# Performance work log

Measured on AMD Instinct MI355X. Metric: run time of the kernel, lower is better.

Reference implementation:

```python
import jax, jax.numpy as jnp
import numpy as np

B, C, H, W = 2, 512, 64, 64
NUM_HEADS = 8
HEAD_DIM = C // NUM_HEADS


def setup_inputs() -> dict:
    key = jax.random.key(0)
    ks = jax.random.split(key, 6)
    s = 1.0 / np.sqrt(C)
    return {
        "x": jax.random.normal(ks[0], (B, C, H, W), dtype=jnp.float32),
        "w_qkv": jax.random.normal(ks[1], (3 * C, C), dtype=jnp.float32) * s,
        "b_qkv": jax.random.normal(ks[2], (3 * C,), dtype=jnp.float32) * 0.01,
        "w_out": jax.random.normal(ks[3], (C, C), dtype=jnp.float32) * s,
        "b_out": jax.random.normal(ks[4], (C,), dtype=jnp.float32) * 0.01,
        "gamma": jax.random.normal(ks[5], (1,), dtype=jnp.float32) * 0.1,
    }


def reference(x, w_qkv, b_qkv, w_out, b_out, gamma):
    b, c, h, w = x.shape
    n = h * w
    nh, hd = NUM_HEADS, HEAD_DIM
    # 1x1 conv QKV projection == per-pixel linear
    qkv = jnp.einsum('oc,bchw->bohw', w_qkv, x) + b_qkv[None, :, None, None]
    qkv = qkv.reshape(b, 3, nh, hd, n)  # [B,3,nh,hd,N]
    q = qkv[:, 0].transpose(0, 1, 3, 2)  # [B,nh,N,hd]
    k = qkv[:, 1]                        # [B,nh,hd,N]
    v = qkv[:, 2].transpose(0, 1, 3, 2)  # [B,nh,N,hd]
    scale = hd ** -0.5
    attn = jnp.einsum('bhnd,bhdm->bhnm', q, k) * scale  # [B,nh,N,N]
    attn = jax.nn.softmax(attn, axis=-1)
    out = jnp.einsum('bhnm,bhmd->bhnd', attn, v)  # [B,nh,N,hd]
    out = out.transpose(0, 1, 3, 2).reshape(b, c, h, w)  # [B,C,H,W]
    out = jnp.einsum('oc,bchw->bohw', w_out, out) + b_out[None, :, None, None]
    return gamma[0] * out + x
```

## Files before the change

kernel.cpp:

```cpp
#include <hip/hip_runtime.h>
#include <hip/hip_bf16.h>

typedef __bf16 bf16_t;
typedef __bf16 bf16x8 __attribute__((ext_vector_type(8)));
typedef __bf16 bf16x4 __attribute__((ext_vector_type(4)));
typedef float floatx4 __attribute__((ext_vector_type(4)));
typedef float f32x16 __attribute__((ext_vector_type(16)));

#define MFMA_BF16(a, b, c) __builtin_amdgcn_mfma_f32_16x16x32_bf16((a), (b), (c), 0, 0, 0)
#define MFMA32(a, b, c) __builtin_amdgcn_mfma_f32_32x32x16_bf16((a), (b), (c), 0, 0, 0)

static constexpr int CB = 512;
static constexpr int NB = 4096;

__device__ __forceinline__ unsigned cvtpk_bf16(float lo, float hi_) {
  unsigned r;
  asm("v_cvt_pk_bf16_f32 %0, %1, %2" : "=v"(r) : "v"(lo), "v"(hi_));
  return r;
}
__device__ __forceinline__ void plswap(unsigned& x, unsigned& y) {
  asm volatile("v_permlane32_swap_b32 %0, %1" : "+v"(x), "+v"(y));
}
__device__ __forceinline__ float exp2_fast(float x) {
  float r;
  asm("v_exp_f32 %0, %1" : "=v"(r) : "v"(x));
  return r;
}

#define GLOAD_LDS16(gsrc, ldst)                                              \
  __builtin_amdgcn_global_load_lds(                                          \
      (const __attribute__((address_space(1))) void*)(gsrc),                 \
      (__attribute__((address_space(3))) void*)(ldst), 16, 0, 0)

__global__ __launch_bounds__(256) void k_transpose(const float* __restrict__ x,
                                                   bf16_t* __restrict__ xT) {
  __shared__ __align__(16) bf16_t T[64 * 72];
  const int t = threadIdx.x;
  const int b = blockIdx.z, c0 = blockIdx.y * 64, n0 = blockIdx.x * 64;
  {
    const int cl = t >> 4, nl = (t & 15) * 4;
#pragma unroll
    for (int p = 0; p < 4; ++p) {
      const int c = cl + p * 16;
      const float4 v = *reinterpret_cast<const float4*>(
          x + ((size_t)(b * CB + c0 + c) * NB) + n0 + nl);
      T[(nl + 0) * 72 + c] = (bf16_t)v.x;
      T[(nl + 1) * 72 + c] = (bf16_t)v.y;
      T[(nl + 2) * 72 + c] = (bf16_t)v.z;
      T[(nl + 3) * 72 + c] = (bf16_t)v.w;
    }
  }
  __syncthreads();
  {
    const int nr = t >> 2, ch = t & 3;
    bf16_t* op = xT + ((size_t)(b * NB + n0 + nr) * CB) + c0;
#pragma unroll
    for (int p = 0; p < 2; ++p) {
      bf16x8 v = *reinterpret_cast<const bf16x8*>(&T[nr * 72 + ch * 8 + p * 32]);
      *reinterpret_cast<bf16x8*>(op + ch * 8 + p * 32) = v;
    }
  }
}

__global__ __launch_bounds__(256) void k_qkv(const float* __restrict__ W,
                                             const float* __restrict__ bias,
                                             const bf16_t* __restrict__ xT,
                                             bf16_t* __restrict__ Qb,
                                             bf16_t* __restrict__ Kb,
                                             bf16_t* __restrict__ Vb) {
  __shared__ __align__(16) bf16_t As[128 * 40];
  __shared__ __align__(16) bf16_t Bs[128 * 40];
  const int t = threadIdx.x;
  const int lane = t & 63, wv = t >> 6;
  const int g = lane >> 4, c = lane & 15;
  const int wm = wv >> 1, wn = wv & 1;
  const int o0 = blockIdx.x * 128, n0 = blockIdx.y * 128;
  const int b = blockIdx.z;

  floatx4 acc[4][4] = {};

  const float* Ap = W + (size_t)o0 * CB;
  const bf16_t* Bp = xT + ((size_t)b * NB + n0) * CB;

  for (int kt = 0; kt < CB; kt += 32) {
    {
      const int row = t >> 3, c4 = (t & 7) * 4;
#pragma unroll
      for (int p = 0; p < 4; ++p) {
        const int r = row + p * 32;
        const float4 v = *reinterpret_cast<const float4*>(Ap + (size_t)r * CB + kt + c4);
        bf16x4 w4;
        w4[0] = (bf16_t)v.x; w4[1] = (bf16_t)v.y; w4[2] = (bf16_t)v.z; w4[3] = (bf16_t)v.w;
        *reinterpret_cast<bf16x4*>(&As[r * 40 + c4]) = w4;
      }
    }
    {
      const int row = t >> 2, ch = t & 3;
#pragma unroll
      for (int p = 0; p < 2; ++p) {
        const int r = row + p * 64;
        bf16x8 v = *reinterpret_cast<const bf16x8*>(Bp + (size_t)r * CB + kt + ch * 8);
        *reinterpret_cast<bf16x8*>(&Bs[r * 40 + ch * 8]) = v;
      }
    }
    __syncthreads();
    bf16x8 af[4], bfr[4];
#pragma unroll
    for (int i = 0; i < 4; ++i)
      af[i] = *reinterpret_cast<const bf16x8*>(&As[(wm * 64 + i * 16 + c) * 40 + g * 8]);
#pragma unroll
    for (int j = 0; j < 4; ++j)
      bfr[j] = *reinterpret_cast<const bf16x8*>(&Bs[(wn * 64 + j * 16 + c) * 40 + g * 8]);
#pragma unroll
    for (int i = 0; i < 4; ++i)
#pragma unroll
      for (int j = 0; j < 4; ++j)
        acc[i][j] = MFMA_BF16(af[i], bfr[j], acc[i][j]);
    __syncthreads();
  }

  const int which = o0 >> 9;
#pragma unroll
  for (int i = 0; i < 4; ++i) {
    const int ob = o0 + wm * 64 + i * 16 + 4 * g;
    float bias4[4];
#pragma unroll
    for (int r = 0; r < 4; ++r) bias4[r] = bias[ob + r];
    const int h = (ob >> 6) & 7;
    const int d0 = ob & 63;
#pragma unroll
    for (int j = 0; j < 4; ++j) {
      const int n = n0 + wn * 64 + j * 16 + c;
      if (which == 2) {
        bf16_t* vp = Vb + (size_t)(b * 8 + h) * 64 * NB + n;
#pragma unroll
        for (int r = 0; r < 4; ++r)
          vp[(size_t)(d0 + r) * NB] = (bf16_t)(acc[i][j][r] + bias4[r]);
      } else {
        bf16_t* qp = (which == 0 ? Qb : Kb) + ((size_t)(b * 8 + h) * NB + n) * 64 + d0;
        bf16x4 pk;
#pragma unroll
        for (int r = 0; r < 4; ++r) pk[r] = (bf16_t)(acc[i][j][r] + bias4[r]);
        *reinterpret_cast<bf16x4*>(qp) = pk;
      }
    }
  }
}

__global__ __launch_bounds__(256, 3) void k_attn(const bf16_t* __restrict__ Qb,
                                                 const bf16_t* __restrict__ Kb,
                                                 const bf16_t* __restrict__ Vb,
                                                 bf16_t* __restrict__ P0,
                                                 bf16_t* __restrict__ P1,
                                                 float* __restrict__ lsum) {
  __shared__ __align__(16) bf16_t Kl[2][4096];
  __shared__ __align__(16) bf16_t Vl[2][4096];
  const int t = threadIdx.x, lane = t & 63, w = t >> 6;
  const int q31 = lane & 31, hi = lane >> 5;

  const int bid = blockIdx.x;
  const int xcd = bid & 7, j = bid >> 3;
  const int bh = xcd * 2 + (j >> 6);
  const int rest = j & 63;
  const int qt = rest >> 1, half = rest & 1;
  const int q0 = qt * 128 + w * 32;
  const int kvbase = half * 2048;

  const size_t base = (size_t)bh * NB * 64;
  const bf16_t* Qp = Qb + base;
  const bf16_t* Kp = Kb + base;
  const bf16_t* Vp = Vb + base;
  bf16_t* Op = (half ? P1 : P0) + base;

  const float SC = 0.125f * 1.44269504088896340736f;
  const float FM = 8.0f;

  bf16x8 qf[4];
#pragma unroll
  for (int ks = 0; ks < 4; ++ks) {
    bf16x8 q = *reinterpret_cast<const bf16x8*>(Qp + (size_t)(q0 + q31) * 64 + ks * 16 + hi * 8);
#pragma unroll
    for (int e = 0; e < 8; ++e) q[e] = (bf16_t)((float)q[e] * SC);
    qf[ks] = q;
  }

  bf16x8 ones;
#pragma unroll
  for (int e = 0; e < 8; ++e) ones[e] = (bf16_t)1.0f;

  const int srow0 = t >> 3, srow1 = srow0 + 32;
  const int sc0 = ((t & 7) ^ (srow0 & 7)) * 8;
  const int sc1 = ((t & 7) ^ (srow1 & 7)) * 8;
  const bf16_t* ksrc0 = Kp + (size_t)(kvbase + srow0) * 64 + sc0;
  const bf16_t* ksrc1 = Kp + (size_t)(kvbase + srow1) * 64 + sc1;
  const bf16_t* vsrc0 = Vp + (size_t)srow0 * NB + kvbase + sc0;
  const bf16_t* vsrc1 = Vp + (size_t)srow1 * NB + kvbase + sc1;

  int c16r[4];
#pragma unroll
  for (int ks = 0; ks < 4; ++ks) c16r[ks] = ((ks * 2 + hi) ^ (q31 & 7)) * 8;

  f32x16 O0 = {}, O1 = {}, lacc = {};
  f32x16 NEGM;
#pragma unroll
  for (int r = 0; r < 16; ++r) NEGM[r] = -FM;

  GLOAD_LDS16(ksrc0, &Kl[0][w * 512]);
  GLOAD_LDS16(ksrc1, &Kl[0][2048 + w * 512]);
  GLOAD_LDS16(vsrc0, &Vl[0][w * 512]);
  GLOAD_LDS16(vsrc1, &Vl[0][2048 + w * 512]);
  __syncthreads();

  for (int s = 0; s < 32; ++s) {
    const bf16_t* Kbuf = &Kl[s & 1][0];
    const bf16_t* Vbuf = &Vl[s & 1][0];
    if (s < 31) {
      const size_t ko = (size_t)(s + 1) * 64 * 64;
      const int vo = (s + 1) * 64;
      bf16_t* kd = &Kl[(s + 1) & 1][0];
      bf16_t* vd = &Vl[(s + 1) & 1][0];
      GLOAD_LDS16(ksrc0 + ko, kd + w * 512);
      GLOAD_LDS16(ksrc1 + ko, kd + 2048 + w * 512);
      GLOAD_LDS16(vsrc0 + vo, vd + w * 512);
      GLOAD_LDS16(vsrc1 + vo, vd + 2048 + w * 512);
    }
    f32x16 st0 = NEGM, st1 = NEGM;
    __builtin_amdgcn_s_setprio(1);
#pragma unroll
    for (int ks = 0; ks < 4; ++ks) {
      bf16x8 kf0 = *reinterpret_cast<const bf16x8*>(&Kbuf[q31 * 64 + c16r[ks]]);
      bf16x8 kf1 = *reinterpret_cast<const bf16x8*>(&Kbuf[(32 + q31) * 64 + c16r[ks]]);
      st0 = MFMA32(kf0, qf[ks], st0);
      st1 = MFMA32(kf1, qf[ks], st1);
    }
    __builtin_amdgcn_s_setprio(0);

#pragma unroll
    for (int r = 0; r < 16; ++r) st0[r] = exp2_fast(st0[r]);
#pragma unroll
    for (int r = 0; r < 16; ++r) st1[r] = exp2_fast(st1[r]);

    __builtin_amdgcn_s_setprio(1);
#pragma unroll
    for (int ks = 0; ks < 4; ++ks) {
      const f32x16& P = (ks < 2) ? st0 : st1;
      const int rb = (ks & 1) * 8;
      unsigned x0 = cvtpk_bf16(P[rb + 0], P[rb + 1]);
      unsigned y0 = cvtpk_bf16(P[rb + 4], P[rb + 5]);
      unsigned x1 = cvtpk_bf16(P[rb + 2], P[rb + 3]);
      unsigned y1 = cvtpk_bf16(P[rb + 6], P[rb + 7]);
      plswap(x0, y0);
      plswap(x1, y1);
      union { unsigned u[4]; bf16x8 v; } pa;
      pa.u[0] = x0; pa.u[1] = x1; pa.u[2] = y0; pa.u[3] = y1;
      bf16x8 vf0 = *reinterpret_cast<const bf16x8*>(&Vbuf[q31 * 64 + c16r[ks]]);
      bf16x8 vf1 = *reinterpret_cast<const bf16x8*>(&Vbuf[(32 + q31) * 64 + c16r[ks]]);
      O0 = MFMA32(pa.v, vf0, O0);
      O1 = MFMA32(pa.v, vf1, O1);
      lacc = MFMA32(pa.v, ones, lacc);
    }
    __builtin_amdgcn_s_setprio(0);
    __syncthreads();
  }

#pragma unroll
  for (int r = 0; r < 16; ++r) {
    const int n = q0 + (r & 3) + 8 * (r >> 2) + 4 * hi;
    bf16_t* op = Op + ((size_t)n) * 64 + q31;
    op[0]  = (bf16_t)O0[r];
    op[32] = (bf16_t)O1[r];
  }
  if (q31 == 0) {
    float* lp = lsum + (size_t)(half * 16 + bh) * NB;
#pragma unroll
    for (int r = 0; r < 16; ++r) {
      const int row = (r & 3) + 8 * (r >> 2) + 4 * hi;
      lp[q0 + row] = lacc[r];
    }
  }
}

__global__ __launch_bounds__(256) void k_rl(const float* __restrict__ lsum,
                                            float* __restrict__ rlb) {
  const int i = blockIdx.x * 256 + threadIdx.x;
  rlb[i] = 1.0f / (lsum[i] + lsum[i + 16 * NB]);
}

__global__ __launch_bounds__(256) void k_out(const float* __restrict__ W,
                                             const float* __restrict__ bias,
                                             const bf16_t* __restrict__ P0,
                                             const bf16_t* __restrict__ P1,
                                             const float* __restrict__ rlb,
                                             const float* __restrict__ x,
                                             const float* __restrict__ gamma,
                                             float* __restrict__ y) {
  __shared__ __align__(16) bf16_t As[128 * 40];
  __shared__ __align__(16) bf16_t Bs[128 * 40];
  const int t = threadIdx.x;
  const int lane = t & 63, wv = t >> 6;
  const int g = lane >> 4, c = lane & 15;
  const int wm = wv >> 1, wn = wv & 1;
  const int o0 = blockIdx.x * 128, n0 = blockIdx.y * 128;
  const int b = blockIdx.z;

  floatx4 acc[4][4] = {};

  const float* Ap = W + (size_t)o0 * CB;

  for (int kt = 0; kt < CB; kt += 32) {
    {
      const int row = t >> 3, c4 = (t & 7) * 4;
#pragma unroll
      for (int p = 0; p < 4; ++p) {
        const int r = row + p * 32;
        const float4 v = *reinterpret_cast<const float4*>(Ap + (size_t)r * CB + kt + c4);
        bf16x4 w4;
        w4[0] = (bf16_t)v.x; w4[1] = (bf16_t)v.y; w4[2] = (bf16_t)v.z; w4[3] = (bf16_t)v.w;
        *reinterpret_cast<bf16x4*>(&As[r * 40 + c4]) = w4;
      }
    }
    {
      const int row = t >> 2, ch = t & 3;
      const int cc = kt + ch * 8;
      const int h = cc >> 6, d = cc & 63;
#pragma unroll
      for (int p = 0; p < 2; ++p) {
        const int r = row + p * 64;
        const int n = n0 + r;
        const size_t idx = ((size_t)(b * 8 + h) * NB + n) * 64 + d;
        const bf16x8 oa = *reinterpret_cast<const bf16x8*>(P0 + idx);
        const bf16x8 ob = *reinterpret_cast<const bf16x8*>(P1 + idx);
        const float rl = rlb[(size_t)(b * 8 + h) * NB + n];
        bf16x8 o;
#pragma unroll
        for (int e = 0; e < 8; ++e)
          o[e] = (bf16_t)(((float)oa[e] + (float)ob[e]) * rl);
        *reinterpret_cast<bf16x8*>(&Bs[r * 40 + ch * 8]) = o;
      }
    }
    __syncthreads();
    bf16x8 af[4], bfr[4];
#pragma unroll
    for (int i = 0; i < 4; ++i)
      af[i] = *reinterpret_cast<const bf16x8*>(&As[(wm * 64 + i * 16 + c) * 40 + g * 8]);
#pragma unroll
    for (int j = 0; j < 4; ++j)
      bfr[j] = *reinterpret_cast<const bf16x8*>(&Bs[(wn * 64 + j * 16 + c) * 40 + g * 8]);
#pragma unroll
    for (int i = 0; i < 4; ++i)
#pragma unroll
      for (int j = 0; j < 4; ++j)
        acc[i][j] = MFMA_BF16(af[i], bfr[j], acc[i][j]);
    __syncthreads();
  }

  const float gm = gamma[0];
#pragma unroll
  for (int i = 0; i < 4; ++i) {
    const int ob = o0 + wm * 64 + i * 16 + 4 * g;
    float bias4[4];
#pragma unroll
    for (int r = 0; r < 4; ++r) bias4[r] = bias[ob + r];
#pragma unroll
    for (int j = 0; j < 4; ++j) {
      const int n = n0 + wn * 64 + j * 16 + c;
      const float* xp = x + ((size_t)(b * CB + ob) * NB) + n;
      float* yp = y + ((size_t)(b * CB + ob) * NB) + n;
#pragma unroll
      for (int r = 0; r < 4; ++r)
        yp[(size_t)r * NB] = gm * (acc[i][j][r] + bias4[r]) + xp[(size_t)r * NB];
    }
  }
}

extern "C" void kernel_launch(void* const* d_in, const int* in_sizes, int n_in,
                              void* d_out, int out_size, void* d_ws, size_t ws_size,
                              hipStream_t stream) {
  const float* x      = (const float*)d_in[0];
  const float* w_qkv  = (const float*)d_in[1];
  const float* b_qkv  = (const float*)d_in[2];
  const float* w_out  = (const float*)d_in[3];
  const float* b_out  = (const float*)d_in[4];
  const float* gamma  = (const float*)d_in[5];
  float* y = (float*)d_out;

  const size_t CH = 4194304;
  bf16_t* Wp = (bf16_t*)d_ws;
  bf16_t* Qb = Wp;
  bf16_t* Kb = Wp + CH;
  bf16_t* Vb = Wp + 2 * CH;
  bf16_t* P0 = Wp + 3 * CH;
  bf16_t* xT = Wp + 4 * CH;
  bf16_t* P1 = Wp + 4 * CH;
  float*  lsum = (float*)(Wp + 5 * CH);
  float*  rlb  = (float*)(Wp + 5 * CH + 262144 * 2);

  k_transpose<<<dim3(64, 8, 2), 256, 0, stream>>>(x, xT);
  k_qkv<<<dim3(12, 32, 2), 256, 0, stream>>>(w_qkv, b_qkv, xT, Qb, Kb, Vb);
  k_attn<<<dim3(1024), 256, 0, stream>>>(Qb, Kb, Vb, P0, P1, lsum);
  k_rl<<<dim3(256), 256, 0, stream>>>(lsum, rlb);
  k_out<<<dim3(4, 32, 2), 256, 0, stream>>>(w_out, b_out, P0, P1, rlb, x, gamma, y);
}
```

Baseline: 155.9 us.

## Triple-buffer K/V tiles in attention and fold reciprocal-sum kernel into output GEMM

The attention kernel moves from double- to triple-buffered K/V LDS tiles, prefetching two tiles ahead. It replaces __syncthreads with explicit vmcnt waits plus raw barriers, so one tile's loads can stay in flight across iterations. The separate k_rl launch is removed and k_out computes the reciprocal of the summed lsum partials inline. LDS per block rises from 32KB to 48KB, which may reduce occupancy at 3 blocks per CU, and the reciprocal is recomputed redundantly across output tiles.

After: 153.9 us. No clear change (-1.3%).

```diff
diff --git a/kernel.cpp b/kernel.cpp
--- a/kernel.cpp
+++ b/kernel.cpp
@@ -153,8 +153,8 @@
                                                  bf16_t* __restrict__ P0,
                                                  bf16_t* __restrict__ P1,
                                                  float* __restrict__ lsum) {
-  __shared__ __align__(16) bf16_t Kl[2][4096];
-  __shared__ __align__(16) bf16_t Vl[2][4096];
+  __shared__ __align__(16) bf16_t Kl[3][4096];
+  __shared__ __align__(16) bf16_t Vl[3][4096];
   const int t = threadIdx.x, lane = t & 63, w = t >> 6;
   const int q31 = lane & 31, hi = lane >> 5;
 
@@ -196,6 +196,18 @@
   const bf16_t* vsrc0 = Vp + (size_t)srow0 * NB + kvbase + sc0;
   const bf16_t* vsrc1 = Vp + (size_t)srow1 * NB + kvbase + sc1;
 
+#define STAGE_TILE(ss, slot)                                                  \
+  do {                                                                        \
+    const size_t ko_ = (size_t)(ss) * 64 * 64;                                \
+    const int vo_ = (ss) * 64;                                                \
+    bf16_t* kd_ = &Kl[(slot)][0];                                             \
+    bf16_t* vd_ = &Vl[(slot)][0];                                             \
+    GLOAD_LDS16(ksrc0 + ko_, kd_ + w * 512);                                  \
+    GLOAD_LDS16(ksrc1 + ko_, kd_ + 2048 + w * 512);                           \
+    GLOAD_LDS16(vsrc0 + vo_, vd_ + w * 512);                                  \
+    GLOAD_LDS16(vsrc1 + vo_, vd_ + 2048 + w * 512);                           \
+  } while (0)
+
   int c16r[4];
 #pragma unroll
   for (int ks = 0; ks < 4; ++ks) c16r[ks] = ((ks * 2 + hi) ^ (q31 & 7)) * 8;
@@ -205,24 +217,19 @@
 #pragma unroll
   for (int r = 0; r < 16; ++r) NEGM[r] = -FM;
 
-  GLOAD_LDS16(ksrc0, &Kl[0][w * 512]);
-  GLOAD_LDS16(ksrc1, &Kl[0][2048 + w * 512]);
-  GLOAD_LDS16(vsrc0, &Vl[0][w * 512]);
-  GLOAD_LDS16(vsrc1, &Vl[0][2048 + w * 512]);
-  __syncthreads();
-
+  STAGE_TILE(0, 0);
+  STAGE_TILE(1, 1);
+  asm volatile("s_waitcnt vmcnt(4)" ::: "memory");
+  __builtin_amdgcn_s_barrier();
+  __builtin_amdgcn_sched_barrier(0);
+
+  int cur = 0;
   for (int s = 0; s < 32; ++s) {
-    const bf16_t* Kbuf = &Kl[s & 1][0];
-    const bf16_t* Vbuf = &Vl[s & 1][0];
-    if (s < 31) {
-      const size_t ko = (size_t)(s + 1) * 64 * 64;
-      const int vo = (s + 1) * 64;
-      bf16_t* kd = &Kl[(s + 1) & 1][0];
-      bf16_t* vd = &Vl[(s + 1) & 1][0];
-      GLOAD_LDS16(ksrc0 + ko, kd + w * 512);
-      GLOAD_LDS16(ksrc1 + ko, kd + 2048 + w * 512);
-      GLOAD_LDS16(vsrc0 + vo, vd + w * 512);
-      GLOAD_LDS16(vsrc1 + vo, vd + 2048 + w * 512);
+    const bf16_t* Kbuf = &Kl[cur][0];
+    const bf16_t* Vbuf = &Vl[cur][0];
+    if (s < 30) {
+      int nx2 = cur + 2; if (nx2 >= 3) nx2 -= 3;
+      STAGE_TILE(s + 2, nx2);
     }
     f32x16 st0 = NEGM, st1 = NEGM;
     __builtin_amdgcn_s_setprio(1);
@@ -260,8 +267,18 @@
       lacc = MFMA32(pa.v, ones, lacc);
     }
     __builtin_amdgcn_s_setprio(0);
-    __syncthreads();
-  }
+
+    if (s < 31) {
+      if (s < 30)
+        asm volatile("s_waitcnt vmcnt(4) lgkmcnt(0)" ::: "memory");
+      else
+        asm volatile("s_waitcnt vmcnt(0) lgkmcnt(0)" ::: "memory");
+      __builtin_amdgcn_s_barrier();
+      __builtin_amdgcn_sched_barrier(0);
+    }
+    ++cur; if (cur >= 3) cur = 0;
+  }
+#undef STAGE_TILE
 
 #pragma unroll
   for (int r = 0; r < 16; ++r) {
@@ -280,17 +297,11 @@
   }
 }
 
-__global__ __launch_bounds__(256) void k_rl(const float* __restrict__ lsum,
-                                            float* __restrict__ rlb) {
-  const int i = blockIdx.x * 256 + threadIdx.x;
-  rlb[i] = 1.0f / (lsum[i] + lsum[i + 16 * NB]);
-}
-
 __global__ __launch_bounds__(256) void k_out(const float* __restrict__ W,
                                              const float* __restrict__ bias,
                                              const bf16_t* __restrict__ P0,
                                              const bf16_t* __restrict__ P1,
-                                             const float* __restrict__ rlb,
+                                             const float* __restrict__ lsum,
                                              const float* __restrict__ x,
                                              const float* __restrict__ gamma,
                                              float* __restrict__ y) {
@@ -327,10 +338,11 @@
       for (int p = 0; p < 2; ++p) {
         const int r = row + p * 64;
         const int n = n0 + r;
-        const size_t idx = ((size_t)(b * 8 + h) * NB + n) * 64 + d;
+        const size_t li = (size_t)(b * 8 + h) * NB + n;
+        const size_t idx = li * 64 + d;
         const bf16x8 oa = *reinterpret_cast<const bf16x8*>(P0 + idx);
         const bf16x8 ob = *reinterpret_cast<const bf16x8*>(P1 + idx);
-        const float rl = rlb[(size_t)(b * 8 + h) * NB + n];
+        const float rl = 1.0f / (lsum[li] + lsum[li + 16 * NB]);
         bf16x8 o;
 #pragma unroll
         for (int e = 0; e < 8; ++e)
@@ -393,11 +405,9 @@
   bf16_t* xT = Wp + 4 * CH;
   bf16_t* P1 = Wp + 4 * CH;
   float*  lsum = (float*)(Wp + 5 * CH);
-  float*  rlb  = (float*)(Wp + 5 * CH + 262144 * 2);
 
   k_transpose<<<dim3(64, 8, 2), 256, 0, stream>>>(x, xT);
   k_qkv<<<dim3(12, 32, 2), 256, 0, stream>>>(w_qkv, b_qkv, xT, Qb, Kb, Vb);
   k_attn<<<dim3(1024), 256, 0, stream>>>(Qb, Kb, Vb, P0, P1, lsum);
-  k_rl<<<dim3(256), 256, 0, stream>>>(lsum, rlb);
-  k_out<<<dim3(4, 32, 2), 256, 0, stream>>>(w_out, b_out, P0, P1, rlb, x, gamma, y);
-}
+  k_out<<<dim3(4, 32, 2), 256, 0, stream>>>(w_out, b_out, P0, P1, lsum, x, gamma, y);
+}
```
